# Optimization experiments

Hardware: AMD Instinct MI355X
Metric: run time of the kernel (lower is better)

## Reference

```python
import jax, jax.numpy as jnp
import numpy as np

SM_SCALE = 0.08838834764831845  # 1/sqrt(128)
SLIDING_WINDOW = 128
N_TOKENS, N_HEADS, Q_MULT, D_HEAD = 2048, 8, 4, 128


def setup_inputs() -> dict:
    key = jax.random.key(0)
    k1, k2, k3, k4 = jax.random.split(key, 4)
    Q = jax.random.normal(k1, (N_TOKENS, N_HEADS, Q_MULT, D_HEAD), dtype=jnp.float32)
    K = jax.random.normal(k2, (N_TOKENS, N_HEADS, D_HEAD), dtype=jnp.float32)
    V = jax.random.normal(k3, (N_TOKENS, N_HEADS, D_HEAD), dtype=jnp.float32)
    S = jax.random.normal(k4, (N_HEADS * Q_MULT,), dtype=jnp.float32)
    return {"Q": Q, "K": K, "V": V, "S": S}


def _build_mask(n_tokens, sliding_window, dtype):
    q_idx = jnp.arange(n_tokens)[:, None]
    k_idx = jnp.arange(n_tokens)[None, :]
    # causal: disallow k > q; sliding window: disallow k <= q - sliding_window
    disallowed = k_idx > q_idx
    if sliding_window > 0:
        disallowed = disallowed | (k_idx <= q_idx - sliding_window)
    return jnp.where(disallowed, jnp.array(-jnp.inf, dtype), jnp.array(0.0, dtype))


def reference(Q, K, V, S):
    n_tokens, n_heads, q_mult, d_head = Q.shape
    mask = _build_mask(n_tokens, SLIDING_WINDOW, Q.dtype)  # (T, T)
    # scores: (h, m, q, k)
    QK = jnp.einsum('qhmd,khd->hmqk', Q, K) * SM_SCALE
    QK = QK + mask[None, None, :, :]
    # append per-(head, q_mult) sink logit as an extra key column
    sink = jnp.broadcast_to(S.reshape(n_heads, q_mult, 1, 1),
                            (n_heads, q_mult, n_tokens, 1))
    QK = jnp.concatenate([QK, sink], axis=-1)  # (h, m, q, k+1)
    W = jax.nn.softmax(QK, axis=-1)[..., :-1]  # drop sink column
    attn = jnp.einsum('hmqk,khd->qhmd', W, V)
    return attn.reshape(n_tokens, n_heads * q_mult * d_head)
```

## Files before the change

### kernel.cpp

```cpp
#include <hip/hip_runtime.h>
#include <cstdint>

#define T_TOK 2048
#define NH 8
#define QM 4
#define DH 128
#define BQ 64
#define ROWS 256
#define CK 32
#define KS 136
#define VS 40
#define PS 40
#define SM_SCALE 0.08838834764831845f

typedef __attribute__((ext_vector_type(8))) short short8v;
typedef __attribute__((ext_vector_type(4))) short short4v;
typedef __attribute__((ext_vector_type(2))) short short2v;
typedef __attribute__((ext_vector_type(4))) float floatx4;

static __device__ __forceinline__ short f2bf(float x) {
  union { float f; unsigned u; } v; v.f = x;
  return (short)((v.u + 0x7fffu + ((v.u >> 16) & 1u)) >> 16);
}

__global__ __launch_bounds__(1024, 4)
void attn_fwd(const float* __restrict__ Qp, const float* __restrict__ Kp,
              const float* __restrict__ Vp, const float* __restrict__ Sp,
              float* __restrict__ Op) {
  __shared__ short k_s[2][CK * KS];
  __shared__ short v_s[2][DH * VS];
  __shared__ short p_s[ROWS * PS];

  const int t    = threadIdx.x;
  const int lane = t & 63;
  const int wv   = t >> 6;
  const int quad = lane >> 4;
  const int l16  = lane & 15;

  const int bx = blockIdx.x;
  const int h  = bx & 7;
  const int q0 = (bx >> 3) * BQ;
  const int lo0 = q0 > 127 ? q0 - 127 : 0;
  const int nk  = q0 + BQ - lo0;
  const int nch = (nk + CK - 1) >> 5;

  const int Ra = wv * 16 + l16;
  const int qa = q0 + (Ra >> 2), ma = Ra & 3;
  const float* qptr = Qp + ((size_t)qa * (NH * QM) + h * QM + ma) * DH + quad * 8;
  short8v qf[4];
#pragma unroll
  for (int s = 0; s < 4; ++s) {
    float4 x0 = *(const float4*)(qptr + 32 * s);
    float4 x1 = *(const float4*)(qptr + 32 * s + 4);
    short8v f;
    f[0] = f2bf(x0.x); f[1] = f2bf(x0.y); f[2] = f2bf(x0.z); f[3] = f2bf(x0.w);
    f[4] = f2bf(x1.x); f[5] = f2bf(x1.y); f[6] = f2bf(x1.z); f[7] = f2bf(x1.w);
    qf[s] = f;
  }

  const int kj  = t >> 5;
  const int kd4 = (t & 31) * 4;
  const int vd  = t & 127;
  const int vg  = t >> 7;

  const int qc = q0 + wv * 4 + quad;
  float dn[4] = {0.f, 0.f, 0.f, 0.f};
  floatx4 oacc[8];
#pragma unroll
  for (int nt = 0; nt < 8; ++nt) oacc[nt] = (floatx4)0.0f;

  float4 pk;
  float  pv[4];
  {
    int g = lo0 + kj; g = g < T_TOK ? g : T_TOK - 1;
    pk = *(const float4*)(Kp + ((size_t)g * NH + h) * DH + kd4);
#pragma unroll
    for (int u = 0; u < 4; ++u) {
      const int s = vg * 4 + u;
      int gk = lo0 + (s >> 1) + ((s & 1) << 4);
      gk = gk < T_TOK ? gk : T_TOK - 1;
      pv[u] = Vp[((size_t)gk * NH + h) * DH + vd];
    }
  }

  for (int c = 0; c < nch; ++c) {
    const int b  = c & 1;
    const int kb = lo0 + c * CK;

    {
      short4v s4;
      s4[0] = f2bf(pk.x); s4[1] = f2bf(pk.y); s4[2] = f2bf(pk.z); s4[3] = f2bf(pk.w);
      *(short4v*)(&k_s[b][kj * KS + kd4]) = s4;
      short4v t4;
      t4[0] = f2bf(pv[0]); t4[1] = f2bf(pv[1]); t4[2] = f2bf(pv[2]); t4[3] = f2bf(pv[3]);
      *(short4v*)(&v_s[b][vd * VS + vg * 4]) = t4;
    }
    __syncthreads();

    if (c + 1 < nch) {
      const int kb2 = kb + CK;
      int g = kb2 + kj; g = g < T_TOK ? g : T_TOK - 1;
      pk = *(const float4*)(Kp + ((size_t)g * NH + h) * DH + kd4);
#pragma unroll
      for (int u = 0; u < 4; ++u) {
        const int s = vg * 4 + u;
        int gk = kb2 + (s >> 1) + ((s & 1) << 4);
        gk = gk < T_TOK ? gk : T_TOK - 1;
        pv[u] = Vp[((size_t)gk * NH + h) * DH + vd];
      }
    }

    floatx4 sc0 = (floatx4)0.0f, sc1 = (floatx4)0.0f;
#pragma unroll
    for (int s = 0; s < 4; ++s) {
      short8v k0 = *(const short8v*)(&k_s[b][l16 * KS + quad * 8 + 32 * s]);
      short8v k1 = *(const short8v*)(&k_s[b][(l16 + 16) * KS + quad * 8 + 32 * s]);
      sc0 = __builtin_amdgcn_mfma_f32_16x16x32_bf16(qf[s], k0, sc0, 0, 0, 0);
      sc1 = __builtin_amdgcn_mfma_f32_16x16x32_bf16(qf[s], k1, sc1, 0, 0, 0);
    }

    const int k0i = kb + l16, k1i = kb + 16 + l16;
    const bool ok0 = (k0i <= qc) && (k0i > qc - 128);
    const bool ok1 = (k1i <= qc) && (k1i > qc - 128);
#pragma unroll
    for (int r = 0; r < 4; ++r) {
      float e0 = ok0 ? __expf(sc0[r] * SM_SCALE) : 0.f;
      float e1 = ok1 ? __expf(sc1[r] * SM_SCALE) : 0.f;
      dn[r] += e0 + e1;
      const int R = wv * 16 + quad * 4 + r;
      short2v p2; p2[0] = f2bf(e0); p2[1] = f2bf(e1);
      *(short2v*)(&p_s[R * PS + 2 * l16]) = p2;
    }

    short8v pf = *(const short8v*)(&p_s[(wv * 16 + l16) * PS + quad * 8]);
#pragma unroll
    for (int nt = 0; nt < 8; ++nt) {
      short8v vf = *(const short8v*)(&v_s[b][(l16 + 16 * nt) * VS + quad * 8]);
      oacc[nt] = __builtin_amdgcn_mfma_f32_16x16x32_bf16(pf, vf, oacc[nt], 0, 0, 0);
    }
  }

#pragma unroll
  for (int r = 0; r < 4; ++r) {
    float s = dn[r];
#pragma unroll
    for (int mm = 1; mm <= 8; mm <<= 1) s += __shfl_xor(s, mm);
    const float total = s + __expf(Sp[h * QM + r]);
    const float rd = 1.0f / total;
    float* ob = Op + (size_t)qc * (NH * QM * DH) + ((size_t)h * QM + r) * DH + l16;
#pragma unroll
    for (int nt = 0; nt < 8; ++nt) ob[nt * 16] = oacc[nt][r] * rd;
  }
}

extern "C" void kernel_launch(void* const* d_in, const int* in_sizes, int n_in,
                              void* d_out, int out_size, void* d_ws, size_t ws_size,
                              hipStream_t stream) {
  const float* Q = (const float*)d_in[0];
  const float* K = (const float*)d_in[1];
  const float* V = (const float*)d_in[2];
  const float* S = (const float*)d_in[3];
  float* O = (float*)d_out;
  const int grid = (T_TOK / BQ) * NH;
  attn_fwd<<<dim3(grid), dim3(1024), 0, stream>>>(Q, K, V, S, O);
}
```

Measured before the change: 103.9 us.

## Preconvert K/V to bf16 in workspace and read MFMA operands directly from global

Adds a preconvert kernel that casts K to bf16 and writes V as a transposed bf16 copy into the workspace. The attention kernel then drops its shared-memory K/V staging, double buffering and block-wide barriers, and loads MFMA operands straight from global (and so from cache). The query block shrinks from 64 to 16 tokens with 256-thread blocks, and the chunk start is aligned to 32, so more, smaller blocks reread K/V through cache. The cost is an extra kernel launch, a workspace round trip, and more redundant global reads of K/V with uncoalesced 16-byte fetches per lane.

```diff
diff --git a/kernel.cpp b/kernel.cpp
--- a/kernel.cpp
+++ b/kernel.cpp
@@ -5,17 +5,12 @@
 #define NH 8
 #define QM 4
 #define DH 128
-#define BQ 64
-#define ROWS 256
-#define CK 32
-#define KS 136
-#define VS 40
+#define NHD 1024
+#define BQ 16
 #define PS 40
 #define SM_SCALE 0.08838834764831845f
 
 typedef __attribute__((ext_vector_type(8))) short short8v;
-typedef __attribute__((ext_vector_type(4))) short short4v;
-typedef __attribute__((ext_vector_type(2))) short short2v;
 typedef __attribute__((ext_vector_type(4))) float floatx4;
 
 static __device__ __forceinline__ short f2bf(float x) {
@@ -23,13 +18,49 @@
   return (short)((v.u + 0x7fffu + ((v.u >> 16) & 1u)) >> 16);
 }
 
-__global__ __launch_bounds__(1024, 4)
-void attn_fwd(const float* __restrict__ Qp, const float* __restrict__ Kp,
-              const float* __restrict__ Vp, const float* __restrict__ Sp,
+__global__ __launch_bounds__(256)
+void preconvert(const float* __restrict__ K, const float* __restrict__ V,
+                short* __restrict__ Kb, short* __restrict__ Vt) {
+  const int b = blockIdx.x, t = threadIdx.x;
+  if (b < 256) {
+    __shared__ short lt[64][130];
+    const int h = b & 7, t0 = (b >> 3) << 6;
+    const int tt = t >> 2, d0 = (t & 3) * 32;
+    const float* src = V + ((size_t)(t0 + tt) * NH + h) * DH + d0;
+#pragma unroll
+    for (int u = 0; u < 8; ++u) {
+      float4 x = *(const float4*)(src + 4 * u);
+      lt[tt][d0 + 4 * u + 0] = f2bf(x.x);
+      lt[tt][d0 + 4 * u + 1] = f2bf(x.y);
+      lt[tt][d0 + 4 * u + 2] = f2bf(x.z);
+      lt[tt][d0 + 4 * u + 3] = f2bf(x.w);
+    }
+    __syncthreads();
+    const int d = t >> 1, half = t & 1;
+    short* dst = Vt + ((size_t)h * DH + d) * T_TOK + t0 + half * 32;
+#pragma unroll
+    for (int w = 0; w < 4; ++w) {
+      short8v o;
+#pragma unroll
+      for (int j = 0; j < 8; ++j) o[j] = lt[half * 32 + w * 8 + j][d];
+      *(short8v*)(dst + w * 8) = o;
+    }
+  } else {
+    const int idx = (b - 256) * 256 + t;
+    const float* src = K + (size_t)idx * 8;
+    float4 a = *(const float4*)src, c = *(const float4*)(src + 4);
+    short8v o;
+    o[0] = f2bf(a.x); o[1] = f2bf(a.y); o[2] = f2bf(a.z); o[3] = f2bf(a.w);
+    o[4] = f2bf(c.x); o[5] = f2bf(c.y); o[6] = f2bf(c.z); o[7] = f2bf(c.w);
+    *(short8v*)(Kb + (size_t)idx * 8) = o;
+  }
+}
+
+__global__ __launch_bounds__(256, 4)
+void attn_fwd(const float* __restrict__ Qp, const short* __restrict__ Kb,
+              const short* __restrict__ Vt, const float* __restrict__ Sp,
               float* __restrict__ Op) {
-  __shared__ short k_s[2][CK * KS];
-  __shared__ short v_s[2][DH * VS];
-  __shared__ short p_s[ROWS * PS];
+  __shared__ short p_s[64 * PS];
 
   const int t    = threadIdx.x;
   const int lane = t & 63;
@@ -40,9 +71,10 @@
   const int bx = blockIdx.x;
   const int h  = bx & 7;
   const int q0 = (bx >> 3) * BQ;
-  const int lo0 = q0 > 127 ? q0 - 127 : 0;
+  int lo0 = q0 > 127 ? q0 - 127 : 0;
+  lo0 &= ~31;
   const int nk  = q0 + BQ - lo0;
-  const int nch = (nk + CK - 1) >> 5;
+  const int nch = (nk + 31) >> 5;
 
   const int Ra = wv * 16 + l16;
   const int qa = q0 + (Ra >> 2), ma = Ra & 3;
@@ -58,63 +90,28 @@
     qf[s] = f;
   }
 
-  const int kj  = t >> 5;
-  const int kd4 = (t & 31) * 4;
-  const int vd  = t & 127;
-  const int vg  = t >> 7;
-
   const int qc = q0 + wv * 4 + quad;
   float dn[4] = {0.f, 0.f, 0.f, 0.f};
   floatx4 oacc[8];
 #pragma unroll
   for (int nt = 0; nt < 8; ++nt) oacc[nt] = (floatx4)0.0f;
 
-  float4 pk;
-  float  pv[4];
-  {
-    int g = lo0 + kj; g = g < T_TOK ? g : T_TOK - 1;
-    pk = *(const float4*)(Kp + ((size_t)g * NH + h) * DH + kd4);
-#pragma unroll
-    for (int u = 0; u < 4; ++u) {
-      const int s = vg * 4 + u;
-      int gk = lo0 + (s >> 1) + ((s & 1) << 4);
-      gk = gk < T_TOK ? gk : T_TOK - 1;
-      pv[u] = Vp[((size_t)gk * NH + h) * DH + vd];
-    }
-  }
+  const short* kbase = Kb + (size_t)h * DH;
+  const short* vbase = Vt + (size_t)h * DH * T_TOK;
 
   for (int c = 0; c < nch; ++c) {
-    const int b  = c & 1;
-    const int kb = lo0 + c * CK;
+    const int kb = lo0 + c * 32;
 
-    {
-      short4v s4;
-      s4[0] = f2bf(pk.x); s4[1] = f2bf(pk.y); s4[2] = f2bf(pk.z); s4[3] = f2bf(pk.w);
-      *(short4v*)(&k_s[b][kj * KS + kd4]) = s4;
-      short4v t4;
-      t4[0] = f2bf(pv[0]); t4[1] = f2bf(pv[1]); t4[2] = f2bf(pv[2]); t4[3] = f2bf(pv[3]);
-      *(short4v*)(&v_s[b][vd * VS + vg * 4]) = t4;
-    }
-    __syncthreads();
-
-    if (c + 1 < nch) {
-      const int kb2 = kb + CK;
-      int g = kb2 + kj; g = g < T_TOK ? g : T_TOK - 1;
-      pk = *(const float4*)(Kp + ((size_t)g * NH + h) * DH + kd4);
-#pragma unroll
-      for (int u = 0; u < 4; ++u) {
-        const int s = vg * 4 + u;
-        int gk = kb2 + (s >> 1) + ((s & 1) << 4);
-        gk = gk < T_TOK ? gk : T_TOK - 1;
-        pv[u] = Vp[((size_t)gk * NH + h) * DH + vd];
-      }
-    }
+    int g0 = kb + l16;      g0 = g0 < T_TOK ? g0 : T_TOK - 1;
+    int g1 = kb + 16 + l16; g1 = g1 < T_TOK ? g1 : T_TOK - 1;
+    const short* kp0 = kbase + (size_t)g0 * NHD + quad * 8;
+    const short* kp1 = kbase + (size_t)g1 * NHD + quad * 8;
 
     floatx4 sc0 = (floatx4)0.0f, sc1 = (floatx4)0.0f;
 #pragma unroll
     for (int s = 0; s < 4; ++s) {
-      short8v k0 = *(const short8v*)(&k_s[b][l16 * KS + quad * 8 + 32 * s]);
-      short8v k1 = *(const short8v*)(&k_s[b][(l16 + 16) * KS + quad * 8 + 32 * s]);
+      short8v k0 = *(const short8v*)(kp0 + 32 * s);
+      short8v k1 = *(const short8v*)(kp1 + 32 * s);
       sc0 = __builtin_amdgcn_mfma_f32_16x16x32_bf16(qf[s], k0, sc0, 0, 0, 0);
       sc1 = __builtin_amdgcn_mfma_f32_16x16x32_bf16(qf[s], k1, sc1, 0, 0, 0);
     }
@@ -128,14 +125,15 @@
       float e1 = ok1 ? __expf(sc1[r] * SM_SCALE) : 0.f;
       dn[r] += e0 + e1;
       const int R = wv * 16 + quad * 4 + r;
-      short2v p2; p2[0] = f2bf(e0); p2[1] = f2bf(e1);
-      *(short2v*)(&p_s[R * PS + 2 * l16]) = p2;
+      p_s[R * PS + l16]      = f2bf(e0);
+      p_s[R * PS + 16 + l16] = f2bf(e1);
     }
+    short8v pf = *(const short8v*)(&p_s[(wv * 16 + l16) * PS + quad * 8]);
 
-    short8v pf = *(const short8v*)(&p_s[(wv * 16 + l16) * PS + quad * 8]);
+    const int vt0 = kb + quad * 8;
 #pragma unroll
     for (int nt = 0; nt < 8; ++nt) {
-      short8v vf = *(const short8v*)(&v_s[b][(l16 + 16 * nt) * VS + quad * 8]);
+      short8v vf = *(const short8v*)(vbase + (size_t)(l16 + 16 * nt) * T_TOK + vt0);
       oacc[nt] = __builtin_amdgcn_mfma_f32_16x16x32_bf16(pf, vf, oacc[nt], 0, 0, 0);
     }
   }
@@ -161,6 +159,10 @@
   const float* V = (const float*)d_in[2];
   const float* S = (const float*)d_in[3];
   float* O = (float*)d_out;
+  short* Kb = (short*)d_ws;
+  short* Vt = Kb + (size_t)T_TOK * NHD;
+
+  preconvert<<<dim3(1280), dim3(256), 0, stream>>>(K, V, Kb, Vt);
   const int grid = (T_TOK / BQ) * NH;
-  attn_fwd<<<dim3(grid), dim3(1024), 0, stream>>>(Q, K, V, S, O);
+  attn_fwd<<<dim3(grid), dim3(256), 0, stream>>>(Q, Kb, Vt, S, O);
 }
```

Result: slower. 134.8 us (+29.7%).
